# Kernel tuning notes

Hardware: AMD Instinct MI355X
Metric: run time of the kernel (lower is better)

Reference implementation:

```python
import jax, jax.numpy as jnp
import numpy as np

B, N, G, E, H, R = 4, 50000, 2, 500000, 64, 16


def setup_inputs() -> dict:
    key = jax.random.key(0)
    ks = jax.random.split(key, 12)
    return {
        "pert_mask": (jax.random.uniform(ks[0], (B, N)) < 0.1).astype(jnp.float32),
        "ctx_emb": jax.random.normal(ks[1], (B, H), jnp.float32),
        "edge_src": jax.random.randint(ks[2], (G, E), 0, N, jnp.int32),
        "edge_dst": jax.random.randint(ks[3], (G, E), 0, N, jnp.int32),
        "edge_weight": jax.random.uniform(ks[4], (G, E), jnp.float32),
        "gate_u": jax.random.normal(ks[5], (G, N, R), jnp.float32) * 0.1,
        "gate_v": jax.random.normal(ks[6], (G, N, R), jnp.float32) * 0.1,
        "lin_w": jax.random.normal(ks[7], (H,), jnp.float32) * 0.1,
        "lin_b": jax.random.normal(ks[8], (H,), jnp.float32) * 0.1,
        "post_w": jax.random.normal(ks[9], (H, H), jnp.float32) * (1.0 / np.sqrt(H)),
        "post_b": jax.random.normal(ks[10], (H,), jnp.float32) * 0.1,
        "mix_w": jax.random.normal(ks[11], (H, G), jnp.float32) * 0.1,
        "mix_b": jnp.zeros((G,), jnp.float32),
    }


def reference(pert_mask, ctx_emb, edge_src, edge_dst, edge_weight,
              gate_u, gate_v, lin_w, lin_b, post_w, post_b, mix_w, mix_b):
    # h0 = Linear(1, H)(pert_mask[..., None])  -> [B, N, H]
    h0 = pert_mask[..., None] * lin_w + lin_b
    h_list = []
    for i in range(edge_src.shape[0]):  # fixed, small number of graphs
        src, dst = edge_src[i], edge_dst[i]
        # low-rank edge gate: sigmoid(<u[src], v[dst]>)  -> [E]
        gate = jax.nn.sigmoid(jnp.sum(gate_u[i][src] * gate_v[i][dst], axis=-1))
        w = edge_weight[i] * gate  # [E]
        # gather -> weight -> scatter-add, batched over B
        msg = h0[:, src, :] * w[None, :, None]  # [B, E, H]
        agg = jnp.zeros_like(h0).at[:, dst, :].add(msg)  # [B, N, H]
        h = jax.nn.relu(agg @ post_w + post_b)  # post Linear + ReLU
        h_list.append(h.mean(axis=1))  # mean over nodes -> [B, H]
    Hs = jnp.stack(h_list, axis=1)  # [B, G, H]
    wts = jax.nn.softmax(ctx_emb @ mix_w + mix_b, axis=1)[..., None]  # [B, G, 1]
    return (Hs * wts).sum(axis=1)  # [B, H]
```

## Files before the change

kernel.cpp:

```cpp
#include <hip/hip_runtime.h>

#define BB 4
#define NN 50000
#define GG 2
#define EE 500000
#define HH 64
#define RR 16

#define CVT (GG * NN)
#define PREPB ((CVT + 255) / 256)

#define NTT   512
#define TILES 98
#define PBLK  128
#define EPB   ((EE + PBLK - 1) / PBLK)
#define CAP   64
#define OVF_MAX 8192

typedef float f32x2 __attribute__((ext_vector_type(2)));

__device__ inline unsigned int pack4_fp8(float f0, float f1, float f2, float f3) {
    int w = 0;
    w = __builtin_amdgcn_cvt_pk_fp8_f32(f0, f1, w, false);
    w = __builtin_amdgcn_cvt_pk_fp8_f32(f2, f3, w, true);
    return (unsigned int)w;
}

__device__ inline float dot16_fp8(uint4 a, uint4 b) {
    const unsigned int* pa = &a.x;
    const unsigned int* pb = &b.x;
    float s = 0.f;
#pragma unroll
    for (int i = 0; i < 4; ++i) {
        f32x2 al = __builtin_amdgcn_cvt_pk_f32_fp8((int)pa[i], false);
        f32x2 ah = __builtin_amdgcn_cvt_pk_f32_fp8((int)pa[i], true);
        f32x2 bl = __builtin_amdgcn_cvt_pk_f32_fp8((int)pb[i], false);
        f32x2 bh = __builtin_amdgcn_cvt_pk_f32_fp8((int)pb[i], true);
        s = fmaf(al.x, bl.x, s);
        s = fmaf(al.y, bl.y, s);
        s = fmaf(ah.x, bh.x, s);
        s = fmaf(ah.y, bh.y, s);
    }
    return s;
}

__device__ inline unsigned int f32_to_bf16_rn(float x) {
    unsigned int u = __float_as_uint(x);
    return (u + 0x7FFFu + ((u >> 16) & 1u)) >> 16;
}

__global__ __launch_bounds__(256) void prep_kernel(
    const float* __restrict__ pert_mask,
    const float* __restrict__ gu, const float* __restrict__ gv,
    uint4* __restrict__ guh, uint4* __restrict__ gvh,
    int* __restrict__ ovf_cnt)
{
    int t = blockIdx.x * 256 + threadIdx.x;
    if (t == 0) *ovf_cnt = 0;
    if (t < CVT) {
        int n = (t >= NN) ? (t - NN) : t;
        const float4* us = (const float4*)(gu + (size_t)t * RR);
        const float4* vs = (const float4*)(gv + (size_t)t * RR);
        float4 a0 = us[0], a1 = us[1], a2 = us[2], a3 = us[3];
        uint4 ur;
        ur.x = pack4_fp8(a0.x, a0.y, a0.z, a0.w);
        ur.y = pack4_fp8(a1.x, a1.y, a1.z, a1.w);
        ur.z = pack4_fp8(a2.x, a2.y, a2.z, a2.w);
        ur.w = pack4_fp8(a3.x, a3.y, a3.z, a3.w);
        unsigned int mbits =
            ((pert_mask[0*NN + n] != 0.f) ? 0x1u        : 0u) |
            ((pert_mask[1*NN + n] != 0.f) ? 0x100u      : 0u) |
            ((pert_mask[2*NN + n] != 0.f) ? 0x10000u    : 0u) |
            ((pert_mask[3*NN + n] != 0.f) ? 0x1000000u  : 0u);
        ur.x = (ur.x & 0xFEFEFEFEu) | mbits;
        guh[t] = ur;
        float4 b0 = vs[0], b1 = vs[1], b2 = vs[2], b3 = vs[3];
        uint4 vr;
        vr.x = pack4_fp8(b0.x, b0.y, b0.z, b0.w);
        vr.y = pack4_fp8(b1.x, b1.y, b1.z, b1.w);
        vr.z = pack4_fp8(b2.x, b2.y, b2.z, b2.w);
        vr.w = pack4_fp8(b3.x, b3.y, b3.z, b3.w);
        gvh[t] = vr;
    }
}

__device__ inline void emit_edge(
    uint4 ua, uint4 va, float w0, int d, int g,
    int* lcnt, unsigned int* __restrict__ bins, int blk,
    int* __restrict__ ovf_cnt, uint2* __restrict__ ovf)
{
    float dot = dot16_fp8(ua, va);
    float w = w0 / (1.f + __expf(-dot));
    unsigned int mb = (ua.x & 1u) | ((ua.x >> 7) & 2u) |
                      ((ua.x >> 14) & 4u) | ((ua.x >> 21) & 8u);
    int tt = d >> 9;
    int dl = d & (NTT - 1);
    int pos = atomicAdd(&lcnt[tt], 1);
    if (pos < CAP) {
        unsigned int rec = (f32_to_bf16_rn(w) << 16) | (mb << 9) | (unsigned)dl;
        bins[(((size_t)g * TILES + tt) * PBLK + blk) * CAP + pos] = rec;
    } else {
        int idx = atomicAdd(ovf_cnt, 1);
        if (idx < OVF_MAX)
            ovf[idx] = make_uint2((unsigned)(g * NN + d) | (mb << 20),
                                  __float_as_uint(w));
    }
}

__global__ __launch_bounds__(256) void edge_bin_kernel(
    const int* __restrict__ esrc, const int* __restrict__ edst,
    const float* __restrict__ ewgt, const uint4* __restrict__ guh,
    const uint4* __restrict__ gvh,
    unsigned int* __restrict__ bins, int* __restrict__ counts,
    int* __restrict__ ovf_cnt, uint2* __restrict__ ovf,
    float* __restrict__ out)
{
    int g   = blockIdx.x & 1;
    int blk = blockIdx.x >> 1;
    __shared__ int lcnt[TILES];
    int tid = threadIdx.x;
    if (tid < TILES) lcnt[tid] = 0;
    if (blockIdx.x == 0 && tid < BB * HH) out[tid] = 0.f;
    __syncthreads();

    int base   = blk * EPB;
    int nEdges = min(EPB, EE - base);
    size_t gbase = (size_t)g * EE + base;
    int gN = g * NN;
    for (int it = tid; it < nEdges; it += 512) {
        int itB = it + 256;
        bool hB = itB < nEdges;
        int itBc = hB ? itB : it;
        int   sA  = __builtin_nontemporal_load(esrc + gbase + it);
        int   dA  = __builtin_nontemporal_load(edst + gbase + it);
        float wA  = __builtin_nontemporal_load(ewgt + gbase + it);
        int   sB  = __builtin_nontemporal_load(esrc + gbase + itBc);
        int   dB  = __builtin_nontemporal_load(edst + gbase + itBc);
        float wB  = __builtin_nontemporal_load(ewgt + gbase + itBc);
        uint4 uA = guh[gN + sA];
        uint4 vA = gvh[gN + dA];
        uint4 uB = guh[gN + sB];
        uint4 vB = gvh[gN + dB];
        emit_edge(uA, vA, wA, dA, g, lcnt, bins, blk, ovf_cnt, ovf);
        if (hB) emit_edge(uB, vB, wB, dB, g, lcnt, bins, blk, ovf_cnt, ovf);
    }
    __syncthreads();
    if (tid < TILES)
        counts[((size_t)g * TILES + tid) * PBLK + blk] = min(lcnt[tid], CAP);
}

#define P2T 1024

__global__ __launch_bounds__(P2T) void tile_node_kernel(
    const unsigned int* __restrict__ bins, const int* __restrict__ counts,
    const float* __restrict__ ctx, const float* __restrict__ lin_w,
    const float* __restrict__ lin_b, const float* __restrict__ post_w,
    const float* __restrict__ post_b, const float* __restrict__ mix_w,
    const float* __restrict__ mix_b,
    const int* __restrict__ ovf_cnt, const uint2* __restrict__ ovf,
    float* __restrict__ out)
{
    int t = blockIdx.x;
    int g = blockIdx.y;
    int n0 = t * NTT;
    int ncnt = min(NTT, NN - n0);
    __shared__ float ls[5][NTT];
    __shared__ int   lcnts[PBLK];
    __shared__ float red[4][BB * HH];
    __shared__ float lpw[HH], lpb[HH], lwt[BB];
    __shared__ int   s_ovfn;
    int tid = threadIdx.x;

    for (int i = tid; i < 5 * NTT; i += P2T) ((float*)ls)[i] = 0.f;
    if (tid < PBLK)
        lcnts[tid] = __builtin_nontemporal_load(
            counts + ((size_t)g * TILES + t) * PBLK + tid);
    if (tid >= P2T - HH) {
        int h = tid - (P2T - HH);
        float a = 0.f, c = 0.f;
        for (int k = 0; k < HH; ++k) {
            float w = post_w[k * HH + h];
            a = fmaf(lin_w[k], w, a);
            c = fmaf(lin_b[k], w, c);
        }
        lpw[h] = a; lpb[h] = c;
    } else if (tid >= P2T - HH - BB) {
        int b = tid - (P2T - HH - BB);
        float l0 = mix_b[0], l1 = mix_b[1];
        for (int h = 0; h < HH; ++h) {
            float cv = ctx[b * HH + h];
            l0 = fmaf(cv, mix_w[h * GG + 0], l0);
            l1 = fmaf(cv, mix_w[h * GG + 1], l1);
        }
        float m = fmaxf(l0, l1);
        float e0 = __expf(l0 - m), e1 = __expf(l1 - m);
        lwt[b] = ((g == 0) ? e0 : e1) / (e0 + e1);
    } else if (tid == 0) {
        s_ovfn = min(*ovf_cnt, OVF_MAX);
    }
    __syncthreads();

    int wv = tid >> 6, ln = tid & 63;
    const unsigned int* bbase = bins + ((size_t)g * TILES + t) * PBLK * CAP;
    for (int bI = wv; bI < PBLK; bI += P2T / 64) {
        int cnt = lcnts[bI];
        const unsigned int* rp = bbase + (size_t)bI * CAP;
        for (int i = ln; i < cnt; i += 64) {
            unsigned int r = __builtin_nontemporal_load(rp + i);
            float w = __uint_as_float(r & 0xFFFF0000u);
            int d = r & (NTT - 1);
            unsigned int mb = (r >> 9) & 15u;
            atomicAdd(&ls[0][d], w);
            if (mb & 1u) atomicAdd(&ls[1][d], w);
            if (mb & 2u) atomicAdd(&ls[2][d], w);
            if (mb & 4u) atomicAdd(&ls[3][d], w);
            if (mb & 8u) atomicAdd(&ls[4][d], w);
        }
    }
    for (int i = tid; i < s_ovfn; i += P2T) {
        uint2 r = ovf[i];
        int key = (int)(r.x & 0xFFFFFu);
        int lo = g * NN + n0;
        if (key >= lo && key < lo + ncnt) {
            int d = key - lo;
            unsigned int mb = (r.x >> 20) & 15u;
            float w = __uint_as_float(r.y);
            atomicAdd(&ls[0][d], w);
            if (mb & 1u) atomicAdd(&ls[1][d], w);
            if (mb & 2u) atomicAdd(&ls[2][d], w);
            if (mb & 4u) atomicAdd(&ls[3][d], w);
            if (mb & 8u) atomicAdd(&ls[4][d], w);
        }
    }
    __syncthreads();

    int b   = (tid >> 6) & 3;
    int sub = tid >> 8;
    int h   = tid & 63;
    float pwh = lpw[h], pbh = lpb[h], bias = post_b[h];
    float acc = 0.f;
    int i0 = sub * (NTT / 4);
    int i1 = min(i0 + (NTT / 4), ncnt);
    for (int i = i0; i < i1; ++i) {
        float x = fmaf(ls[1 + b][i], pwh, fmaf(ls[0][i], pbh, bias));
        acc += fmaxf(x, 0.f);
    }
    red[sub][b * HH + h] = acc;
    __syncthreads();
    if (tid < BB * HH) {
        float s = red[0][tid] + red[1][tid] + red[2][tid] + red[3][tid];
        int bb = tid >> 6;
        atomicAdd(&out[tid], s * lwt[bb] * (1.0f / NN));
    }
}

extern "C" void kernel_launch(void* const* d_in, const int* in_sizes, int n_in,
                              void* d_out, int out_size, void* d_ws, size_t ws_size,
                              hipStream_t stream) {
    const float* pert_mask = (const float*)d_in[0];
    const float* ctx       = (const float*)d_in[1];
    const int*   esrc      = (const int*)d_in[2];
    const int*   edst      = (const int*)d_in[3];
    const float* ewgt      = (const float*)d_in[4];
    const float* gu        = (const float*)d_in[5];
    const float* gv        = (const float*)d_in[6];
    const float* lin_w     = (const float*)d_in[7];
    const float* lin_b     = (const float*)d_in[8];
    const float* post_w    = (const float*)d_in[9];
    const float* post_b    = (const float*)d_in[10];
    const float* mix_w     = (const float*)d_in[11];
    const float* mix_b     = (const float*)d_in[12];
    float* out = (float*)d_out;

    float* ws = (float*)d_ws;
    uint4* guh = (uint4*)ws;
    uint4* gvh = guh + 100000;
    unsigned int* bins = (unsigned int*)(ws + 800000);
    int* counts = (int*)(bins + (size_t)GG * TILES * PBLK * CAP);
    int* ovf_cnt = counts + GG * TILES * PBLK;
    uint2* ovf = (uint2*)(ovf_cnt + 2);

    prep_kernel<<<PREPB, 256, 0, stream>>>(
        pert_mask, gu, gv, guh, gvh, ovf_cnt);

    edge_bin_kernel<<<2 * PBLK, 256, 0, stream>>>(
        esrc, edst, ewgt, guh, gvh, bins, counts, ovf_cnt, ovf, out);

    dim3 tg(TILES, GG);
    tile_node_kernel<<<tg, P2T, 0, stream>>>(
        bins, counts, ctx, lin_w, lin_b, post_w, post_b, mix_w, mix_b,
        ovf_cnt, ovf, out);
}
```

Before: 56.39 us.

## Fuse prep into binning and defer edge gate computation to tile kernel

Merges the gate_u fp8 packing into the edge-binning kernel, removing one launch and the gate_v conversion pass. Bins now hold raw (src, dst, weight) 64-bit records instead of precomputed gated bf16 weights. The tile kernel stages its tile's gate_v rows in fp32 LDS and computes the sigmoid gate at accumulation time. The global overflow buffer is replaced by per-block spill regions that every tile scans with a range check. This doubles bin record size and moves the random guh gathers and gate math into the tile kernel, trading extra memory traffic there for one fewer launch and less prep work.

```diff
diff --git a/kernel.cpp b/kernel.cpp
--- a/kernel.cpp
+++ b/kernel.cpp
@@ -8,14 +8,14 @@
 #define RR 16
 
 #define CVT (GG * NN)
-#define PREPB ((CVT + 255) / 256)
+#define K1B 256
+#define ROWS_PB ((CVT + K1B - 1) / K1B)
 
 #define NTT   512
 #define TILES 98
 #define PBLK  128
 #define EPB   ((EE + PBLK - 1) / PBLK)
 #define CAP   64
-#define OVF_MAX 8192
 
 typedef float f32x2 __attribute__((ext_vector_type(2)));
 
@@ -26,41 +26,29 @@
     return (unsigned int)w;
 }
 
-__device__ inline float dot16_fp8(uint4 a, uint4 b) {
-    const unsigned int* pa = &a.x;
-    const unsigned int* pb = &b.x;
-    float s = 0.f;
-#pragma unroll
-    for (int i = 0; i < 4; ++i) {
-        f32x2 al = __builtin_amdgcn_cvt_pk_f32_fp8((int)pa[i], false);
-        f32x2 ah = __builtin_amdgcn_cvt_pk_f32_fp8((int)pa[i], true);
-        f32x2 bl = __builtin_amdgcn_cvt_pk_f32_fp8((int)pb[i], false);
-        f32x2 bh = __builtin_amdgcn_cvt_pk_f32_fp8((int)pb[i], true);
-        s = fmaf(al.x, bl.x, s);
-        s = fmaf(al.y, bl.y, s);
-        s = fmaf(ah.x, bh.x, s);
-        s = fmaf(ah.y, bh.y, s);
-    }
-    return s;
-}
-
-__device__ inline unsigned int f32_to_bf16_rn(float x) {
-    unsigned int u = __float_as_uint(x);
-    return (u + 0x7FFFu + ((u >> 16) & 1u)) >> 16;
-}
-
-__global__ __launch_bounds__(256) void prep_kernel(
-    const float* __restrict__ pert_mask,
-    const float* __restrict__ gu, const float* __restrict__ gv,
-    uint4* __restrict__ guh, uint4* __restrict__ gvh,
-    int* __restrict__ ovf_cnt)
+__global__ __launch_bounds__(256) void prep_bin_kernel(
+    const float* __restrict__ pert_mask, const float* __restrict__ gu,
+    const int* __restrict__ esrc, const int* __restrict__ edst,
+    const float* __restrict__ ewgt,
+    uint4* __restrict__ guh, unsigned long long* __restrict__ bins,
+    int* __restrict__ counts, unsigned long long* __restrict__ spill,
+    int* __restrict__ scnt, float* __restrict__ out)
 {
-    int t = blockIdx.x * 256 + threadIdx.x;
-    if (t == 0) *ovf_cnt = 0;
-    if (t < CVT) {
-        int n = (t >= NN) ? (t - NN) : t;
-        const float4* us = (const float4*)(gu + (size_t)t * RR);
-        const float4* vs = (const float4*)(gv + (size_t)t * RR);
+    int g   = blockIdx.x & 1;
+    int blk = blockIdx.x >> 1;
+    int tid = threadIdx.x;
+    __shared__ int lcnt[TILES];
+    __shared__ int lspill;
+    if (tid < TILES) lcnt[tid] = 0;
+    if (tid == 0) lspill = 0;
+    if (blockIdx.x == 0 && tid < BB * HH) out[tid] = 0.f;
+    __syncthreads();
+
+    int r0 = blockIdx.x * ROWS_PB;
+    int r1 = min(r0 + ROWS_PB, CVT);
+    for (int r = r0 + tid; r < r1; r += 256) {
+        int n = (r >= NN) ? (r - NN) : r;
+        const float4* us = (const float4*)(gu + (size_t)r * RR);
         float4 a0 = us[0], a1 = us[1], a2 = us[2], a3 = us[3];
         uint4 ur;
         ur.x = pack4_fp8(a0.x, a0.y, a0.z, a0.w);
@@ -73,104 +61,97 @@
             ((pert_mask[2*NN + n] != 0.f) ? 0x10000u    : 0u) |
             ((pert_mask[3*NN + n] != 0.f) ? 0x1000000u  : 0u);
         ur.x = (ur.x & 0xFEFEFEFEu) | mbits;
-        guh[t] = ur;
-        float4 b0 = vs[0], b1 = vs[1], b2 = vs[2], b3 = vs[3];
-        uint4 vr;
-        vr.x = pack4_fp8(b0.x, b0.y, b0.z, b0.w);
-        vr.y = pack4_fp8(b1.x, b1.y, b1.z, b1.w);
-        vr.z = pack4_fp8(b2.x, b2.y, b2.z, b2.w);
-        vr.w = pack4_fp8(b3.x, b3.y, b3.z, b3.w);
-        gvh[t] = vr;
-    }
-}
-
-__device__ inline void emit_edge(
-    uint4 ua, uint4 va, float w0, int d, int g,
-    int* lcnt, unsigned int* __restrict__ bins, int blk,
-    int* __restrict__ ovf_cnt, uint2* __restrict__ ovf)
-{
-    float dot = dot16_fp8(ua, va);
-    float w = w0 / (1.f + __expf(-dot));
-    unsigned int mb = (ua.x & 1u) | ((ua.x >> 7) & 2u) |
-                      ((ua.x >> 14) & 4u) | ((ua.x >> 21) & 8u);
-    int tt = d >> 9;
-    int dl = d & (NTT - 1);
-    int pos = atomicAdd(&lcnt[tt], 1);
-    if (pos < CAP) {
-        unsigned int rec = (f32_to_bf16_rn(w) << 16) | (mb << 9) | (unsigned)dl;
-        bins[(((size_t)g * TILES + tt) * PBLK + blk) * CAP + pos] = rec;
-    } else {
-        int idx = atomicAdd(ovf_cnt, 1);
-        if (idx < OVF_MAX)
-            ovf[idx] = make_uint2((unsigned)(g * NN + d) | (mb << 20),
-                                  __float_as_uint(w));
-    }
-}
-
-__global__ __launch_bounds__(256) void edge_bin_kernel(
-    const int* __restrict__ esrc, const int* __restrict__ edst,
-    const float* __restrict__ ewgt, const uint4* __restrict__ guh,
-    const uint4* __restrict__ gvh,
-    unsigned int* __restrict__ bins, int* __restrict__ counts,
-    int* __restrict__ ovf_cnt, uint2* __restrict__ ovf,
-    float* __restrict__ out)
-{
-    int g   = blockIdx.x & 1;
-    int blk = blockIdx.x >> 1;
-    __shared__ int lcnt[TILES];
-    int tid = threadIdx.x;
-    if (tid < TILES) lcnt[tid] = 0;
-    if (blockIdx.x == 0 && tid < BB * HH) out[tid] = 0.f;
-    __syncthreads();
+        guh[r] = ur;
+    }
 
     int base   = blk * EPB;
-    int nEdges = min(EPB, EE - base);
-    size_t gbase = (size_t)g * EE + base;
-    int gN = g * NN;
-    for (int it = tid; it < nEdges; it += 512) {
-        int itB = it + 256;
-        bool hB = itB < nEdges;
-        int itBc = hB ? itB : it;
-        int   sA  = __builtin_nontemporal_load(esrc + gbase + it);
-        int   dA  = __builtin_nontemporal_load(edst + gbase + it);
-        float wA  = __builtin_nontemporal_load(ewgt + gbase + it);
-        int   sB  = __builtin_nontemporal_load(esrc + gbase + itBc);
-        int   dB  = __builtin_nontemporal_load(edst + gbase + itBc);
-        float wB  = __builtin_nontemporal_load(ewgt + gbase + itBc);
-        uint4 uA = guh[gN + sA];
-        uint4 vA = gvh[gN + dA];
-        uint4 uB = guh[gN + sB];
-        uint4 vB = gvh[gN + dB];
-        emit_edge(uA, vA, wA, dA, g, lcnt, bins, blk, ovf_cnt, ovf);
-        if (hB) emit_edge(uB, vB, wB, dB, g, lcnt, bins, blk, ovf_cnt, ovf);
+    int nE     = min(EPB, EE - base);
+    size_t gb  = (size_t)g * EE + base;
+    for (int it = tid; it < nE; it += 256) {
+        int   s  = __builtin_nontemporal_load(esrc + gb + it);
+        int   d  = __builtin_nontemporal_load(edst + gb + it);
+        float w0 = __builtin_nontemporal_load(ewgt + gb + it);
+        unsigned long long rec =
+            (unsigned long long)((unsigned)s | ((unsigned)d << 16)) |
+            ((unsigned long long)__float_as_uint(w0) << 32);
+        int tt  = d >> 9;
+        int pos = atomicAdd(&lcnt[tt], 1);
+        if (pos < CAP) {
+            bins[(((size_t)g * TILES + tt) * PBLK + blk) * CAP + pos] = rec;
+        } else {
+            int sp = atomicAdd(&lspill, 1);
+            spill[((size_t)g * PBLK + blk) * EPB + sp] = rec;
+        }
     }
     __syncthreads();
     if (tid < TILES)
         counts[((size_t)g * TILES + tid) * PBLK + blk] = min(lcnt[tid], CAP);
+    if (tid == 0) scnt[g * PBLK + blk] = lspill;
 }
 
 #define P2T 1024
 
+__device__ inline void replay_rec(
+    unsigned long long rec, int n0, int ncnt, int g,
+    const uint4* __restrict__ guh, float (*vt)[RR + 1], float (*ls)[NTT],
+    bool check_range)
+{
+    unsigned int key = (unsigned int)rec;
+    int d = (int)(key >> 16);
+    int dl = d - n0;
+    if (check_range && ((unsigned)dl >= (unsigned)ncnt)) return;
+    int s = key & 0xFFFFu;
+    float w0 = __uint_as_float((unsigned int)(rec >> 32));
+    uint4 u = guh[(size_t)g * NN + s];
+    const unsigned int* pu = &u.x;
+    float dot = 0.f;
+#pragma unroll
+    for (int q = 0; q < 4; ++q) {
+        f32x2 lo = __builtin_amdgcn_cvt_pk_f32_fp8((int)pu[q], false);
+        f32x2 hi = __builtin_amdgcn_cvt_pk_f32_fp8((int)pu[q], true);
+        dot = fmaf(lo.x, vt[dl][q * 4 + 0], dot);
+        dot = fmaf(lo.y, vt[dl][q * 4 + 1], dot);
+        dot = fmaf(hi.x, vt[dl][q * 4 + 2], dot);
+        dot = fmaf(hi.y, vt[dl][q * 4 + 3], dot);
+    }
+    float w = w0 / (1.f + __expf(-dot));
+    unsigned int mb = (u.x & 1u) | ((u.x >> 7) & 2u) |
+                      ((u.x >> 14) & 4u) | ((u.x >> 21) & 8u);
+    atomicAdd(&ls[0][dl], w);
+    if (mb & 1u) atomicAdd(&ls[1][dl], w);
+    if (mb & 2u) atomicAdd(&ls[2][dl], w);
+    if (mb & 4u) atomicAdd(&ls[3][dl], w);
+    if (mb & 8u) atomicAdd(&ls[4][dl], w);
+}
+
 __global__ __launch_bounds__(P2T) void tile_node_kernel(
-    const unsigned int* __restrict__ bins, const int* __restrict__ counts,
+    const uint4* __restrict__ guh, const unsigned long long* __restrict__ bins,
+    const int* __restrict__ counts, const unsigned long long* __restrict__ spill,
+    const int* __restrict__ scnt, const float* __restrict__ gv,
     const float* __restrict__ ctx, const float* __restrict__ lin_w,
     const float* __restrict__ lin_b, const float* __restrict__ post_w,
     const float* __restrict__ post_b, const float* __restrict__ mix_w,
-    const float* __restrict__ mix_b,
-    const int* __restrict__ ovf_cnt, const uint2* __restrict__ ovf,
-    float* __restrict__ out)
+    const float* __restrict__ mix_b, float* __restrict__ out)
 {
     int t = blockIdx.x;
     int g = blockIdx.y;
     int n0 = t * NTT;
     int ncnt = min(NTT, NN - n0);
+    __shared__ float vt[NTT][RR + 1];
     __shared__ float ls[5][NTT];
     __shared__ int   lcnts[PBLK];
     __shared__ float red[4][BB * HH];
     __shared__ float lpw[HH], lpb[HH], lwt[BB];
-    __shared__ int   s_ovfn;
     int tid = threadIdx.x;
 
+    for (int i = tid; i < ncnt * 4; i += P2T) {
+        int row = i >> 2, q = i & 3;
+        float4 v = ((const float4*)(gv + ((size_t)g * NN + n0 + row) * RR))[q];
+        vt[row][q * 4 + 0] = v.x;
+        vt[row][q * 4 + 1] = v.y;
+        vt[row][q * 4 + 2] = v.z;
+        vt[row][q * 4 + 3] = v.w;
+    }
     for (int i = tid; i < 5 * NTT; i += P2T) ((float*)ls)[i] = 0.f;
     if (tid < PBLK)
         lcnts[tid] = __builtin_nontemporal_load(
@@ -195,41 +176,27 @@
         float m = fmaxf(l0, l1);
         float e0 = __expf(l0 - m), e1 = __expf(l1 - m);
         lwt[b] = ((g == 0) ? e0 : e1) / (e0 + e1);
-    } else if (tid == 0) {
-        s_ovfn = min(*ovf_cnt, OVF_MAX);
     }
     __syncthreads();
 
     int wv = tid >> 6, ln = tid & 63;
-    const unsigned int* bbase = bins + ((size_t)g * TILES + t) * PBLK * CAP;
+    const unsigned long long* bbase =
+        bins + ((size_t)g * TILES + t) * PBLK * CAP;
+
     for (int bI = wv; bI < PBLK; bI += P2T / 64) {
         int cnt = lcnts[bI];
-        const unsigned int* rp = bbase + (size_t)bI * CAP;
+        const unsigned long long* rp = bbase + (size_t)bI * CAP;
         for (int i = ln; i < cnt; i += 64) {
-            unsigned int r = __builtin_nontemporal_load(rp + i);
-            float w = __uint_as_float(r & 0xFFFF0000u);
-            int d = r & (NTT - 1);
-            unsigned int mb = (r >> 9) & 15u;
-            atomicAdd(&ls[0][d], w);
-            if (mb & 1u) atomicAdd(&ls[1][d], w);
-            if (mb & 2u) atomicAdd(&ls[2][d], w);
-            if (mb & 4u) atomicAdd(&ls[3][d], w);
-            if (mb & 8u) atomicAdd(&ls[4][d], w);
-        }
-    }
-    for (int i = tid; i < s_ovfn; i += P2T) {
-        uint2 r = ovf[i];
-        int key = (int)(r.x & 0xFFFFFu);
-        int lo = g * NN + n0;
-        if (key >= lo && key < lo + ncnt) {
-            int d = key - lo;
-            unsigned int mb = (r.x >> 20) & 15u;
-            float w = __uint_as_float(r.y);
-            atomicAdd(&ls[0][d], w);
-            if (mb & 1u) atomicAdd(&ls[1][d], w);
-            if (mb & 2u) atomicAdd(&ls[2][d], w);
-            if (mb & 4u) atomicAdd(&ls[3][d], w);
-            if (mb & 8u) atomicAdd(&ls[4][d], w);
+            unsigned long long rec = __builtin_nontemporal_load(rp + i);
+            replay_rec(rec, n0, ncnt, g, guh, vt, ls, false);
+        }
+    }
+    for (int bI = wv; bI < PBLK; bI += P2T / 64) {
+        int sc = scnt[g * PBLK + bI];
+        const unsigned long long* rp = spill + ((size_t)g * PBLK + bI) * EPB;
+        for (int i = ln; i < sc; i += 64) {
+            unsigned long long rec = rp[i];
+            replay_rec(rec, n0, ncnt, g, guh, vt, ls, true);
         }
     }
     __syncthreads();
@@ -274,20 +241,16 @@
 
     float* ws = (float*)d_ws;
     uint4* guh = (uint4*)ws;
-    uint4* gvh = guh + 100000;
-    unsigned int* bins = (unsigned int*)(ws + 800000);
-    int* counts = (int*)(bins + (size_t)GG * TILES * PBLK * CAP);
-    int* ovf_cnt = counts + GG * TILES * PBLK;
-    uint2* ovf = (uint2*)(ovf_cnt + 2);
-
-    prep_kernel<<<PREPB, 256, 0, stream>>>(
-        pert_mask, gu, gv, guh, gvh, ovf_cnt);
-
-    edge_bin_kernel<<<2 * PBLK, 256, 0, stream>>>(
-        esrc, edst, ewgt, guh, gvh, bins, counts, ovf_cnt, ovf, out);
+    unsigned long long* bins = (unsigned long long*)(ws + 400000);
+    int* counts = (int*)(ws + 3611264);
+    int* scnt   = (int*)(ws + 3636352);
+    unsigned long long* spill = (unsigned long long*)(ws + 3636608);
+
+    prep_bin_kernel<<<K1B, 256, 0, stream>>>(
+        pert_mask, gu, esrc, edst, ewgt, guh, bins, counts, spill, scnt, out);
 
     dim3 tg(TILES, GG);
     tile_node_kernel<<<tg, P2T, 0, stream>>>(
-        bins, counts, ctx, lin_w, lin_b, post_w, post_b, mix_w, mix_b,
-        ovf_cnt, ovf, out);
-}
+        guh, bins, counts, spill, scnt, gv, ctx, lin_w, lin_b, post_w,
+        post_b, mix_w, mix_b, out);
+}
```

Measured after the change: 49.99 us (median of 2 runs). 1.13x faster.
